# Performance work log

Measured on AMD Instinct MI355X. Metric: run time of the kernel, lower is better.

## Reference

```python
import jax, jax.numpy as jnp
import numpy as np

B, N, L, ND = 512, 4096, 128, 1


def setup_inputs() -> dict:
    key = jax.random.key(0)
    ks = jax.random.split(key, 20)
    g = lambda k, shape, s=0.05: jax.random.normal(k, shape, dtype=jnp.float32) * s
    IN = 3 * L + ND  # MLP input: [mem, mem, delta_t, x]
    inp = {
        "x": jax.random.normal(ks[0], (B, N, ND), jnp.float32),
        "memory": jax.random.normal(ks[1], (N, L), jnp.float32),
        "delta_t": jax.random.normal(ks[2], (B, N, L), jnp.float32),
        "src_w1": g(ks[3], (L, IN)), "src_b1": g(ks[4], (L,)),
        "src_w2": g(ks[5], (L, L)), "src_b2": g(ks[6], (L,)),
        "tar_w1": g(ks[7], (L, IN)), "tar_b1": g(ks[8], (L,)),
        "tar_w2": g(ks[9], (L, L)), "tar_b2": g(ks[10], (L,)),
        "gru_wih": g(ks[11], (3 * L, L)), "gru_whh": g(ks[12], (3 * L, L)),
        "gru_bih": g(ks[13], (3 * L,)), "gru_bhh": g(ks[14], (3 * L,)),
        "source": jax.random.randint(ks[15], (B, 1), 0, N, dtype=jnp.int64),
        "target": jax.random.randint(ks[16], (B, 1), 0, N, dtype=jnp.int64),
    }
    return inp


def _mlp(h, w1, b1, w2, b2):
    return jax.nn.relu(h @ w1.T + b1) @ w2.T + b2


def _gru_cell(inp, h, wih, whh, bih, bhh):
    gi = inp @ wih.T + bih          # [n, 3L]
    gh = h @ whh.T + bhh            # [n, 3L]
    i_r, i_z, i_n = jnp.split(gi, 3, axis=-1)
    h_r, h_z, h_n = jnp.split(gh, 3, axis=-1)
    r = jax.nn.sigmoid(i_r + h_r)
    z = jax.nn.sigmoid(i_z + h_z)
    n = jnp.tanh(i_n + r * h_n)
    return (1.0 - z) * n + z * h


def reference(x, memory, delta_t, src_w1, src_b1, src_w2, src_b2,
              tar_w1, tar_b1, tar_w2, tar_b2,
              gru_wih, gru_whh, gru_bih, gru_bhh, source, target):
    b = x.shape[0]
    bi = jnp.arange(b)
    s = source[:, 0]
    t = target[:, 0]
    src_mem = memory[s]                 # [B, L]
    tar_mem = memory[t]                 # [B, L]
    src_x = x[bi, s, :]                 # [B, ND]
    tar_x = x[bi, t, :]
    src_dt = delta_t[bi, s, :]          # [B, L]
    tar_dt = delta_t[bi, t, :]
    src_in = jnp.concatenate([src_mem, tar_mem, src_dt, src_x], axis=-1)
    tar_in = jnp.concatenate([tar_mem, src_mem, tar_dt, tar_x], axis=-1)
    src_msg = _mlp(src_in, src_w1, src_b1, src_w2, src_b2)
    tar_msg = _mlp(tar_in, tar_w1, tar_b1, tar_w2, tar_b2)

    # unique + scatter_mean == segment-mean over node ids, touching only seen nodes
    ids = jnp.concatenate([s, t], axis=0)                       # [2B]
    msgs = jnp.concatenate([src_msg, tar_msg], axis=0)          # [2B, L]
    n_nodes = memory.shape[0]
    msg_sum = jax.ops.segment_sum(msgs, ids, num_segments=n_nodes)
    cnt = jax.ops.segment_sum(jnp.ones((ids.shape[0],), msgs.dtype), ids,
                              num_segments=n_nodes)
    agg = msg_sum / jnp.maximum(cnt, 1.0)[:, None]              # [N, L]
    new_mem = _gru_cell(agg, memory, gru_wih, gru_whh, gru_bih, gru_bhh)
    seen = (cnt > 0)[:, None]
    return jnp.where(seen, new_mem, memory)
```

## Files before the change

### kernel.cpp

```cpp
#include <hip/hip_runtime.h>
#include <math.h>

#define BB 512
#define NN 4096
#define LL 128
#define IN_DIM 385
#define NK4_1 97
#define NK4_2 32
#define EPB 2
#define GPB 4

#define OFF_MSG   0
#define OFF_CNT   (OFF_MSG + NN * LL)
#define OFF_COUNT (OFF_CNT + NN)
#define OFF_LIST  (OFF_COUNT + 4)
#define OFF_W1PS  529416
#define OFF_W1PT  (OFF_W1PS + NK4_1 * LL * 4)
#define OFF_W2PS  (OFF_W1PT + NK4_1 * LL * 4)
#define OFF_W2PT  (OFF_W2PS + NK4_2 * LL * 4)
#define OFF_WIHP  (OFF_W2PT + NK4_2 * LL * 4)
#define OFF_WHHP  (OFF_WIHP + 3 * NK4_2 * LL * 4)

__global__ __launch_bounds__(256) void prep_kernel(
    const float* __restrict__ sw1, const float* __restrict__ tw1,
    const float* __restrict__ sw2, const float* __restrict__ tw2,
    const float* __restrict__ wih, const float* __restrict__ whh,
    float* __restrict__ ws)
{
    const int i = blockIdx.x * 256 + threadIdx.x;
    const int stride = gridDim.x * 256;

    float4* msg4 = (float4*)(ws + OFF_MSG);
    const float4 z4 = make_float4(0.f, 0.f, 0.f, 0.f);
    for (int idx = i; idx < NN * LL / 4; idx += stride)
        msg4[idx] = z4;
    for (int idx = i; idx < NN; idx += stride)
        ws[OFF_CNT + idx] = 0.0f;
    if (i == 0)
        ((int*)ws)[OFF_COUNT] = 0;

    float4* w1ps = (float4*)(ws + OFF_W1PS);
    float4* w1pt = (float4*)(ws + OFF_W1PT);
    for (int idx = i; idx < NK4_1 * LL; idx += stride) {
        const int k4 = idx >> 7, j = idx & 127;
        const int k = k4 * 4;
        float4 a, b;
        a.x = sw1[j * IN_DIM + k];     b.x = tw1[j * IN_DIM + k];
        a.y = (k + 1 < IN_DIM) ? sw1[j * IN_DIM + k + 1] : 0.f;
        b.y = (k + 1 < IN_DIM) ? tw1[j * IN_DIM + k + 1] : 0.f;
        a.z = (k + 2 < IN_DIM) ? sw1[j * IN_DIM + k + 2] : 0.f;
        b.z = (k + 2 < IN_DIM) ? tw1[j * IN_DIM + k + 2] : 0.f;
        a.w = (k + 3 < IN_DIM) ? sw1[j * IN_DIM + k + 3] : 0.f;
        b.w = (k + 3 < IN_DIM) ? tw1[j * IN_DIM + k + 3] : 0.f;
        w1ps[idx] = a; w1pt[idx] = b;
    }
    float4* w2ps = (float4*)(ws + OFF_W2PS);
    float4* w2pt = (float4*)(ws + OFF_W2PT);
    for (int idx = i; idx < NK4_2 * LL; idx += stride) {
        const int k4 = idx >> 7, j = idx & 127;
        const int k = k4 * 4;
        w2ps[idx] = make_float4(sw2[j * LL + k], sw2[j * LL + k + 1],
                                sw2[j * LL + k + 2], sw2[j * LL + k + 3]);
        w2pt[idx] = make_float4(tw2[j * LL + k], tw2[j * LL + k + 1],
                                tw2[j * LL + k + 2], tw2[j * LL + k + 3]);
    }
    float4* wihp = (float4*)(ws + OFF_WIHP);
    float4* whhp = (float4*)(ws + OFF_WHHP);
    for (int idx = i; idx < 3 * NK4_2 * LL; idx += stride) {
        const int j = idx & 127;
        const int gk = idx >> 7;
        const int gate = gk >> 5, k4 = gk & 31;
        const int row = gate * LL + j, k = k4 * 4;
        wihp[idx] = make_float4(wih[row * LL + k], wih[row * LL + k + 1],
                                wih[row * LL + k + 2], wih[row * LL + k + 3]);
        whhp[idx] = make_float4(whh[row * LL + k], whh[row * LL + k + 1],
                                whh[row * LL + k + 2], whh[row * LL + k + 3]);
    }
}

__global__ __launch_bounds__(256) void edge_msg_kernel(
    const float* __restrict__ x,
    const float* __restrict__ memory,
    const float* __restrict__ delta_t,
    const float* __restrict__ sb1, const float* __restrict__ sb2,
    const float* __restrict__ tb1, const float* __restrict__ tb2,
    const int* __restrict__ source, const int* __restrict__ target,
    float* __restrict__ ws, float* __restrict__ out)
{
    const int tid = threadIdx.x;

    if (blockIdx.x >= 512) {
        const int cb = blockIdx.x - 512;
        float4* out4 = (float4*)out;
        const float4* mem4 = (const float4*)memory;
        for (int idx = cb * 256 + tid; idx < NN * LL / 4; idx += 32 * 256)
            out4[idx] = mem4[idx];
        return;
    }

    const int side  = blockIdx.x & 1;
    const int chunk = blockIdx.x >> 1;
    const int g     = tid >> 7;
    const int j     = tid & 127;

    const int eg0 = chunk * EPB, eg1 = eg0 + 1;
    const int s0 = source[eg0], t0 = target[eg0];
    const int s1 = source[eg1], t1 = target[eg1];
    const int node0  = side ? t0 : s0, other0 = side ? s0 : t0;
    const int node1  = side ? t1 : s1, other1 = side ? s1 : t1;

    __shared__ float h1[LL][EPB];
    __shared__ float part1[2][EPB][LL];
    __shared__ float part2[2][EPB][LL];

    const float4* w1p = (const float4*)(ws + (side ? OFF_W1PT : OFF_W1PS));
    const float4* w2p = (const float4*)(ws + (side ? OFF_W2PT : OFF_W2PS));
    const float* b1  = side ? tb1 : sb1;
    const float* b2  = side ? tb2 : sb2;

    {
        float a0 = 0.f, a1 = 0.f;
        const float* dA = delta_t + ((size_t)eg0 * NN + node0) * LL;
        const float* dB = delta_t + ((size_t)eg1 * NN + node1) * LL;
        if (g == 0) {
            const float* pA = memory + (size_t)node0 * LL;
            const float* pB = memory + (size_t)node1 * LL;
            #pragma unroll 4
            for (int k4 = 0; k4 < 32; ++k4) {
                const float4 w  = w1p[k4 * LL + j];
                const float4 iA = *(const float4*)(pA + 4 * k4);
                const float4 iB = *(const float4*)(pB + 4 * k4);
                a0 = fmaf(w.x, iA.x, a0); a1 = fmaf(w.x, iB.x, a1);
                a0 = fmaf(w.y, iA.y, a0); a1 = fmaf(w.y, iB.y, a1);
                a0 = fmaf(w.z, iA.z, a0); a1 = fmaf(w.z, iB.z, a1);
                a0 = fmaf(w.w, iA.w, a0); a1 = fmaf(w.w, iB.w, a1);
            }
            #pragma unroll 4
            for (int k4 = 64; k4 < 80; ++k4) {
                const float4 w  = w1p[k4 * LL + j];
                const float4 iA = *(const float4*)(dA + 4 * (k4 - 64));
                const float4 iB = *(const float4*)(dB + 4 * (k4 - 64));
                a0 = fmaf(w.x, iA.x, a0); a1 = fmaf(w.x, iB.x, a1);
                a0 = fmaf(w.y, iA.y, a0); a1 = fmaf(w.y, iB.y, a1);
                a0 = fmaf(w.z, iA.z, a0); a1 = fmaf(w.z, iB.z, a1);
                a0 = fmaf(w.w, iA.w, a0); a1 = fmaf(w.w, iB.w, a1);
            }
        } else {
            const float* pA = memory + (size_t)other0 * LL;
            const float* pB = memory + (size_t)other1 * LL;
            #pragma unroll 4
            for (int k4 = 32; k4 < 64; ++k4) {
                const float4 w  = w1p[k4 * LL + j];
                const float4 iA = *(const float4*)(pA + 4 * (k4 - 32));
                const float4 iB = *(const float4*)(pB + 4 * (k4 - 32));
                a0 = fmaf(w.x, iA.x, a0); a1 = fmaf(w.x, iB.x, a1);
                a0 = fmaf(w.y, iA.y, a0); a1 = fmaf(w.y, iB.y, a1);
                a0 = fmaf(w.z, iA.z, a0); a1 = fmaf(w.z, iB.z, a1);
                a0 = fmaf(w.w, iA.w, a0); a1 = fmaf(w.w, iB.w, a1);
            }
            #pragma unroll 4
            for (int k4 = 80; k4 < 96; ++k4) {
                const float4 w  = w1p[k4 * LL + j];
                const float4 iA = *(const float4*)(dA + 4 * (k4 - 64));
                const float4 iB = *(const float4*)(dB + 4 * (k4 - 64));
                a0 = fmaf(w.x, iA.x, a0); a1 = fmaf(w.x, iB.x, a1);
                a0 = fmaf(w.y, iA.y, a0); a1 = fmaf(w.y, iB.y, a1);
                a0 = fmaf(w.z, iA.z, a0); a1 = fmaf(w.z, iB.z, a1);
                a0 = fmaf(w.w, iA.w, a0); a1 = fmaf(w.w, iB.w, a1);
            }
            {
                const float4 w = w1p[96 * LL + j];
                const float xA = x[(size_t)eg0 * NN + node0];
                const float xB = x[(size_t)eg1 * NN + node1];
                a0 = fmaf(w.x, xA, a0);
                a1 = fmaf(w.x, xB, a1);
            }
        }
        part1[g][0][j] = a0;
        part1[g][1][j] = a1;
    }
    __syncthreads();

    h1[j][g] = fmaxf(part1[0][g][j] + part1[1][g][j] + b1[j], 0.0f);
    __syncthreads();

    {
        const int k40 = g * 16, k41 = k40 + 16;
        float a0 = 0.f, a1 = 0.f;
        #pragma unroll 4
        for (int k4 = k40; k4 < k41; ++k4) {
            const float4 w  = w2p[k4 * LL + j];
            const float4 h0 = *(const float4*)&h1[k4 * 4][0];
            const float4 h2 = *(const float4*)&h1[k4 * 4 + 2][0];
            a0 = fmaf(w.x, h0.x, a0); a1 = fmaf(w.x, h0.y, a1);
            a0 = fmaf(w.y, h0.z, a0); a1 = fmaf(w.y, h0.w, a1);
            a0 = fmaf(w.z, h2.x, a0); a1 = fmaf(w.z, h2.y, a1);
            a0 = fmaf(w.w, h2.z, a0); a1 = fmaf(w.w, h2.w, a1);
        }
        part2[g][0][j] = a0;
        part2[g][1][j] = a1;
    }
    __syncthreads();

    {
        const int node = g ? node1 : node0;
        const float m = part2[0][g][j] + part2[1][g][j] + b2[j];
        atomicAdd(ws + OFF_MSG + (size_t)node * LL + j, m);
    }
    if (tid < EPB) {
        const int node = tid ? node1 : node0;
        const float old = atomicAdd(ws + OFF_CNT + node, 1.0f);
        if (old == 0.0f) {
            const int pos = atomicAdd((int*)ws + OFF_COUNT, 1);
            ((int*)ws)[OFF_LIST + pos] = node;
        }
    }
}

__global__ __launch_bounds__(256) void gru_kernel(
    const float* __restrict__ memory,
    const float* __restrict__ bih, const float* __restrict__ bhh,
    const float* __restrict__ ws,
    float* __restrict__ out)
{
    const int tid = threadIdx.x;
    const int g = tid >> 7, j = tid & 127;
    const int scount = ((const int*)ws)[OFF_COUNT];
    const int base = blockIdx.x * GPB;
    if (base >= scount) return;
    const int nact = min(GPB, scount - base);

    __shared__ float gates[6][GPB][LL];
    __shared__ int   nodes_sh[GPB];

    int nd[GPB];
    #pragma unroll
    for (int s = 0; s < GPB; ++s)
        nd[s] = (base + s < scount) ? ((const int*)ws)[OFF_LIST + base + s]
                                    : ((const int*)ws)[OFF_LIST + base];
    if (tid < GPB) nodes_sh[tid] = nd[tid];

    const float* op0; const float* op1; const float* op2; const float* op3;
    float rc0 = 1.f, rc1 = 1.f, rc2 = 1.f, rc3 = 1.f;
    if (g == 0) {
        op0 = ws + OFF_MSG + (size_t)nd[0] * LL;
        op1 = ws + OFF_MSG + (size_t)nd[1] * LL;
        op2 = ws + OFF_MSG + (size_t)nd[2] * LL;
        op3 = ws + OFF_MSG + (size_t)nd[3] * LL;
        rc0 = 1.0f / ws[OFF_CNT + nd[0]];
        rc1 = 1.0f / ws[OFF_CNT + nd[1]];
        rc2 = 1.0f / ws[OFF_CNT + nd[2]];
        rc3 = 1.0f / ws[OFF_CNT + nd[3]];
    } else {
        op0 = memory + (size_t)nd[0] * LL;
        op1 = memory + (size_t)nd[1] * LL;
        op2 = memory + (size_t)nd[2] * LL;
        op3 = memory + (size_t)nd[3] * LL;
    }

    const float4* wp = (const float4*)(ws + (g ? OFF_WHHP : OFF_WIHP));
    float a0[GPB] = {}, a1[GPB] = {}, a2[GPB] = {};
    #pragma unroll 2
    for (int k4 = 0; k4 < NK4_2; ++k4) {
        const float4 w0 = wp[(0 * NK4_2 + k4) * LL + j];
        const float4 w1 = wp[(1 * NK4_2 + k4) * LL + j];
        const float4 w2 = wp[(2 * NK4_2 + k4) * LL + j];
        const float4 v0 = *(const float4*)(op0 + 4 * k4);
        const float4 v1 = *(const float4*)(op1 + 4 * k4);
        const float4 v2 = *(const float4*)(op2 + 4 * k4);
        const float4 v3 = *(const float4*)(op3 + 4 * k4);
        a0[0] = fmaf(w0.x, v0.x, a0[0]); a0[0] = fmaf(w0.y, v0.y, a0[0]);
        a0[0] = fmaf(w0.z, v0.z, a0[0]); a0[0] = fmaf(w0.w, v0.w, a0[0]);
        a1[0] = fmaf(w1.x, v0.x, a1[0]); a1[0] = fmaf(w1.y, v0.y, a1[0]);
        a1[0] = fmaf(w1.z, v0.z, a1[0]); a1[0] = fmaf(w1.w, v0.w, a1[0]);
        a2[0] = fmaf(w2.x, v0.x, a2[0]); a2[0] = fmaf(w2.y, v0.y, a2[0]);
        a2[0] = fmaf(w2.z, v0.z, a2[0]); a2[0] = fmaf(w2.w, v0.w, a2[0]);

        a0[1] = fmaf(w0.x, v1.x, a0[1]); a0[1] = fmaf(w0.y, v1.y, a0[1]);
        a0[1] = fmaf(w0.z, v1.z, a0[1]); a0[1] = fmaf(w0.w, v1.w, a0[1]);
        a1[1] = fmaf(w1.x, v1.x, a1[1]); a1[1] = fmaf(w1.y, v1.y, a1[1]);
        a1[1] = fmaf(w1.z, v1.z, a1[1]); a1[1] = fmaf(w1.w, v1.w, a1[1]);
        a2[1] = fmaf(w2.x, v1.x, a2[1]); a2[1] = fmaf(w2.y, v1.y, a2[1]);
        a2[1] = fmaf(w2.z, v1.z, a2[1]); a2[1] = fmaf(w2.w, v1.w, a2[1]);

        a0[2] = fmaf(w0.x, v2.x, a0[2]); a0[2] = fmaf(w0.y, v2.y, a0[2]);
        a0[2] = fmaf(w0.z, v2.z, a0[2]); a0[2] = fmaf(w0.w, v2.w, a0[2]);
        a1[2] = fmaf(w1.x, v2.x, a1[2]); a1[2] = fmaf(w1.y, v2.y, a1[2]);
        a1[2] = fmaf(w1.z, v2.z, a1[2]); a1[2] = fmaf(w1.w, v2.w, a1[2]);
        a2[2] = fmaf(w2.x, v2.x, a2[2]); a2[2] = fmaf(w2.y, v2.y, a2[2]);
        a2[2] = fmaf(w2.z, v2.z, a2[2]); a2[2] = fmaf(w2.w, v2.w, a2[2]);

        a0[3] = fmaf(w0.x, v3.x, a0[3]); a0[3] = fmaf(w0.y, v3.y, a0[3]);
        a0[3] = fmaf(w0.z, v3.z, a0[3]); a0[3] = fmaf(w0.w, v3.w, a0[3]);
        a1[3] = fmaf(w1.x, v3.x, a1[3]); a1[3] = fmaf(w1.y, v3.y, a1[3]);
        a1[3] = fmaf(w1.z, v3.z, a1[3]); a1[3] = fmaf(w1.w, v3.w, a1[3]);
        a2[3] = fmaf(w2.x, v3.x, a2[3]); a2[3] = fmaf(w2.y, v3.y, a2[3]);
        a2[3] = fmaf(w2.z, v3.z, a2[3]); a2[3] = fmaf(w2.w, v3.w, a2[3]);
    }
    if (g == 0) {
        a0[0] *= rc0; a1[0] *= rc0; a2[0] *= rc0;
        a0[1] *= rc1; a1[1] *= rc1; a2[1] *= rc1;
        a0[2] *= rc2; a1[2] *= rc2; a2[2] *= rc2;
        a0[3] *= rc3; a1[3] *= rc3; a2[3] *= rc3;
    }
    #pragma unroll
    for (int s = 0; s < GPB; ++s) {
        gates[g * 3 + 0][s][j] = a0[s];
        gates[g * 3 + 1][s][j] = a1[s];
        gates[g * 3 + 2][s][j] = a2[s];
    }
    __syncthreads();

    const int total = nact * LL;
    for (int o = tid; o < total; o += 256) {
        const int s = o >> 7, jj = o & 127;
        const int node = nodes_sh[s];
        const float ir = gates[0][s][jj] + bih[jj];
        const float iz = gates[1][s][jj] + bih[LL + jj];
        const float inn = gates[2][s][jj] + bih[2 * LL + jj];
        const float hr = gates[3][s][jj] + bhh[jj];
        const float hz = gates[4][s][jj] + bhh[LL + jj];
        const float hn = gates[5][s][jj] + bhh[2 * LL + jj];
        const float r = 1.0f / (1.0f + __expf(-(ir + hr)));
        const float z = 1.0f / (1.0f + __expf(-(iz + hz)));
        const float n = tanhf(inn + r * hn);
        const float h = memory[(size_t)node * LL + jj];
        out[(size_t)node * LL + jj] = (1.0f - z) * n + z * h;
    }
}

extern "C" void kernel_launch(void* const* d_in, const int* in_sizes, int n_in,
                              void* d_out, int out_size, void* d_ws, size_t ws_size,
                              hipStream_t stream) {
    const float* x        = (const float*)d_in[0];
    const float* memory   = (const float*)d_in[1];
    const float* delta_t  = (const float*)d_in[2];
    const float* src_w1   = (const float*)d_in[3];
    const float* src_b1   = (const float*)d_in[4];
    const float* src_w2   = (const float*)d_in[5];
    const float* src_b2   = (const float*)d_in[6];
    const float* tar_w1   = (const float*)d_in[7];
    const float* tar_b1   = (const float*)d_in[8];
    const float* tar_w2   = (const float*)d_in[9];
    const float* tar_b2   = (const float*)d_in[10];
    const float* gru_wih  = (const float*)d_in[11];
    const float* gru_whh  = (const float*)d_in[12];
    const float* gru_bih  = (const float*)d_in[13];
    const float* gru_bhh  = (const float*)d_in[14];
    const int*   source   = (const int*)d_in[15];
    const int*   target   = (const int*)d_in[16];

    float* out = (float*)d_out;
    float* ws  = (float*)d_ws;

    prep_kernel<<<512, 256, 0, stream>>>(
        src_w1, tar_w1, src_w2, tar_w2, gru_wih, gru_whh, ws);

    edge_msg_kernel<<<544, 256, 0, stream>>>(
        x, memory, delta_t, src_b1, src_b2, tar_b1, tar_b2,
        source, target, ws, out);

    gru_kernel<<<1024 / GPB, 256, 0, stream>>>(
        memory, gru_bih, gru_bhh, ws, out);
}
```

Measured before the change: 35.68 us.

## Widen edge and GRU blocks to 512 threads and move GRU weight packing

Result: slower. 36.80 us (+3.1%).

```diff
diff --git a/kernel.cpp b/kernel.cpp
--- a/kernel.cpp
+++ b/kernel.cpp
@@ -24,7 +24,6 @@
 __global__ __launch_bounds__(256) void prep_kernel(
     const float* __restrict__ sw1, const float* __restrict__ tw1,
     const float* __restrict__ sw2, const float* __restrict__ tw2,
-    const float* __restrict__ wih, const float* __restrict__ whh,
     float* __restrict__ ws)
 {
     const int i = blockIdx.x * 256 + threadIdx.x;
@@ -64,37 +63,46 @@
         w2pt[idx] = make_float4(tw2[j * LL + k], tw2[j * LL + k + 1],
                                 tw2[j * LL + k + 2], tw2[j * LL + k + 3]);
     }
-    float4* wihp = (float4*)(ws + OFF_WIHP);
-    float4* whhp = (float4*)(ws + OFF_WHHP);
-    for (int idx = i; idx < 3 * NK4_2 * LL; idx += stride) {
-        const int j = idx & 127;
-        const int gk = idx >> 7;
-        const int gate = gk >> 5, k4 = gk & 31;
-        const int row = gate * LL + j, k = k4 * 4;
-        wihp[idx] = make_float4(wih[row * LL + k], wih[row * LL + k + 1],
-                                wih[row * LL + k + 2], wih[row * LL + k + 3]);
-        whhp[idx] = make_float4(whh[row * LL + k], whh[row * LL + k + 1],
-                                whh[row * LL + k + 2], whh[row * LL + k + 3]);
-    }
 }
 
-__global__ __launch_bounds__(256) void edge_msg_kernel(
+#define STEP(w, iA, iB)                                   \
+    a0 = fmaf((w).x, (iA).x, a0); a1 = fmaf((w).x, (iB).x, a1); \
+    a0 = fmaf((w).y, (iA).y, a0); a1 = fmaf((w).y, (iB).y, a1); \
+    a0 = fmaf((w).z, (iA).z, a0); a1 = fmaf((w).z, (iB).z, a1); \
+    a0 = fmaf((w).w, (iA).w, a0); a1 = fmaf((w).w, (iB).w, a1);
+
+__global__ __launch_bounds__(512) void edge_msg_kernel(
     const float* __restrict__ x,
     const float* __restrict__ memory,
     const float* __restrict__ delta_t,
     const float* __restrict__ sb1, const float* __restrict__ sb2,
     const float* __restrict__ tb1, const float* __restrict__ tb2,
+    const float* __restrict__ wih, const float* __restrict__ whh,
     const int* __restrict__ source, const int* __restrict__ target,
     float* __restrict__ ws, float* __restrict__ out)
 {
     const int tid = threadIdx.x;
 
     if (blockIdx.x >= 512) {
-        const int cb = blockIdx.x - 512;
-        float4* out4 = (float4*)out;
-        const float4* mem4 = (const float4*)memory;
-        for (int idx = cb * 256 + tid; idx < NN * LL / 4; idx += 32 * 256)
-            out4[idx] = mem4[idx];
+        if (blockIdx.x < 528) {
+            const int cb = blockIdx.x - 512;
+            float4* out4 = (float4*)out;
+            const float4* mem4 = (const float4*)memory;
+            for (int idx = cb * 512 + tid; idx < NN * LL / 4; idx += 16 * 512)
+                out4[idx] = mem4[idx];
+        } else {
+            const int idx = (blockIdx.x - 528) * 512 + tid;
+            const int j = idx & 127;
+            const int gk = idx >> 7;
+            const int gate = gk >> 5, k4 = gk & 31;
+            const int row = gate * LL + j, k = k4 * 4;
+            ((float4*)(ws + OFF_WIHP))[idx] =
+                make_float4(wih[row * LL + k], wih[row * LL + k + 1],
+                            wih[row * LL + k + 2], wih[row * LL + k + 3]);
+            ((float4*)(ws + OFF_WHHP))[idx] =
+                make_float4(whh[row * LL + k], whh[row * LL + k + 1],
+                            whh[row * LL + k + 2], whh[row * LL + k + 3]);
+        }
         return;
     }
 
@@ -110,8 +118,8 @@
     const int node1  = side ? t1 : s1, other1 = side ? s1 : t1;
 
     __shared__ float h1[LL][EPB];
-    __shared__ float part1[2][EPB][LL];
-    __shared__ float part2[2][EPB][LL];
+    __shared__ float part1[4][EPB][LL];
+    __shared__ float part2[4][EPB][LL];
 
     const float4* w1p = (const float4*)(ws + (side ? OFF_W1PT : OFF_W1PS));
     const float4* w2p = (const float4*)(ws + (side ? OFF_W2PT : OFF_W2PS));
@@ -120,60 +128,63 @@
 
     {
         float a0 = 0.f, a1 = 0.f;
+        const float* nA = memory + (size_t)node0 * LL;
+        const float* nB = memory + (size_t)node1 * LL;
+        const float* oA = memory + (size_t)other0 * LL;
+        const float* oB = memory + (size_t)other1 * LL;
         const float* dA = delta_t + ((size_t)eg0 * NN + node0) * LL;
         const float* dB = delta_t + ((size_t)eg1 * NN + node1) * LL;
+
         if (g == 0) {
-            const float* pA = memory + (size_t)node0 * LL;
-            const float* pB = memory + (size_t)node1 * LL;
-            #pragma unroll 4
-            for (int k4 = 0; k4 < 32; ++k4) {
-                const float4 w  = w1p[k4 * LL + j];
-                const float4 iA = *(const float4*)(pA + 4 * k4);
-                const float4 iB = *(const float4*)(pB + 4 * k4);
-                a0 = fmaf(w.x, iA.x, a0); a1 = fmaf(w.x, iB.x, a1);
-                a0 = fmaf(w.y, iA.y, a0); a1 = fmaf(w.y, iB.y, a1);
-                a0 = fmaf(w.z, iA.z, a0); a1 = fmaf(w.z, iB.z, a1);
-                a0 = fmaf(w.w, iA.w, a0); a1 = fmaf(w.w, iB.w, a1);
-            }
-            #pragma unroll 4
-            for (int k4 = 64; k4 < 80; ++k4) {
-                const float4 w  = w1p[k4 * LL + j];
+            #pragma unroll 4
+            for (int k4 = 0; k4 < 24; ++k4) {
+                const float4 w = w1p[k4 * LL + j];
+                const float4 iA = *(const float4*)(nA + 4 * k4);
+                const float4 iB = *(const float4*)(nB + 4 * k4);
+                STEP(w, iA, iB)
+            }
+        } else if (g == 1) {
+            #pragma unroll 4
+            for (int k4 = 24; k4 < 32; ++k4) {
+                const float4 w = w1p[k4 * LL + j];
+                const float4 iA = *(const float4*)(nA + 4 * k4);
+                const float4 iB = *(const float4*)(nB + 4 * k4);
+                STEP(w, iA, iB)
+            }
+            #pragma unroll 4
+            for (int k4 = 32; k4 < 48; ++k4) {
+                const float4 w = w1p[k4 * LL + j];
+                const float4 iA = *(const float4*)(oA + 4 * (k4 - 32));
+                const float4 iB = *(const float4*)(oB + 4 * (k4 - 32));
+                STEP(w, iA, iB)
+            }
+        } else if (g == 2) {
+            #pragma unroll 4
+            for (int k4 = 48; k4 < 64; ++k4) {
+                const float4 w = w1p[k4 * LL + j];
+                const float4 iA = *(const float4*)(oA + 4 * (k4 - 32));
+                const float4 iB = *(const float4*)(oB + 4 * (k4 - 32));
+                STEP(w, iA, iB)
+            }
+            #pragma unroll 4
+            for (int k4 = 64; k4 < 72; ++k4) {
+                const float4 w = w1p[k4 * LL + j];
                 const float4 iA = *(const float4*)(dA + 4 * (k4 - 64));
                 const float4 iB = *(const float4*)(dB + 4 * (k4 - 64));
-                a0 = fmaf(w.x, iA.x, a0); a1 = fmaf(w.x, iB.x, a1);
-                a0 = fmaf(w.y, iA.y, a0); a1 = fmaf(w.y, iB.y, a1);
-                a0 = fmaf(w.z, iA.z, a0); a1 = fmaf(w.z, iB.z, a1);
-                a0 = fmaf(w.w, iA.w, a0); a1 = fmaf(w.w, iB.w, a1);
+                STEP(w, iA, iB)
             }
         } else {
-            const float* pA = memory + (size_t)other0 * LL;
-            const float* pB = memory + (size_t)other1 * LL;
-            #pragma unroll 4
-            for (int k4 = 32; k4 < 64; ++k4) {
-                const float4 w  = w1p[k4 * LL + j];
-                const float4 iA = *(const float4*)(pA + 4 * (k4 - 32));
-                const float4 iB = *(const float4*)(pB + 4 * (k4 - 32));
-                a0 = fmaf(w.x, iA.x, a0); a1 = fmaf(w.x, iB.x, a1);
-                a0 = fmaf(w.y, iA.y, a0); a1 = fmaf(w.y, iB.y, a1);
-                a0 = fmaf(w.z, iA.z, a0); a1 = fmaf(w.z, iB.z, a1);
-                a0 = fmaf(w.w, iA.w, a0); a1 = fmaf(w.w, iB.w, a1);
-            }
-            #pragma unroll 4
-            for (int k4 = 80; k4 < 96; ++k4) {
-                const float4 w  = w1p[k4 * LL + j];
+            #pragma unroll 4
+            for (int k4 = 72; k4 < 96; ++k4) {
+                const float4 w = w1p[k4 * LL + j];
                 const float4 iA = *(const float4*)(dA + 4 * (k4 - 64));
                 const float4 iB = *(const float4*)(dB + 4 * (k4 - 64));
-                a0 = fmaf(w.x, iA.x, a0); a1 = fmaf(w.x, iB.x, a1);
-                a0 = fmaf(w.y, iA.y, a0); a1 = fmaf(w.y, iB.y, a1);
-                a0 = fmaf(w.z, iA.z, a0); a1 = fmaf(w.z, iB.z, a1);
-                a0 = fmaf(w.w, iA.w, a0); a1 = fmaf(w.w, iB.w, a1);
+                STEP(w, iA, iB)
             }
             {
                 const float4 w = w1p[96 * LL + j];
-                const float xA = x[(size_t)eg0 * NN + node0];
-                const float xB = x[(size_t)eg1 * NN + node1];
-                a0 = fmaf(w.x, xA, a0);
-                a1 = fmaf(w.x, xB, a1);
+                a0 = fmaf(w.x, x[(size_t)eg0 * NN + node0], a0);
+                a1 = fmaf(w.x, x[(size_t)eg1 * NN + node1], a1);
             }
         }
         part1[g][0][j] = a0;
@@ -181,11 +192,15 @@
     }
     __syncthreads();
 
-    h1[j][g] = fmaxf(part1[0][g][j] + part1[1][g][j] + b1[j], 0.0f);
+    if (g < EPB) {
+        const float v = part1[0][g][j] + part1[1][g][j]
+                      + part1[2][g][j] + part1[3][g][j] + b1[j];
+        h1[j][g] = fmaxf(v, 0.0f);
+    }
     __syncthreads();
 
     {
-        const int k40 = g * 16, k41 = k40 + 16;
+        const int k40 = g * 8, k41 = k40 + 8;
         float a0 = 0.f, a1 = 0.f;
         #pragma unroll 4
         for (int k4 = k40; k4 < k41; ++k4) {
@@ -202,9 +217,10 @@
     }
     __syncthreads();
 
-    {
+    if (g < EPB) {
         const int node = g ? node1 : node0;
-        const float m = part2[0][g][j] + part2[1][g][j] + b2[j];
+        const float m = part2[0][g][j] + part2[1][g][j]
+                      + part2[2][g][j] + part2[3][g][j] + b2[j];
         atomicAdd(ws + OFF_MSG + (size_t)node * LL + j, m);
     }
     if (tid < EPB) {
@@ -217,20 +233,20 @@
     }
 }
 
-__global__ __launch_bounds__(256) void gru_kernel(
+__global__ __launch_bounds__(512) void gru_kernel(
     const float* __restrict__ memory,
     const float* __restrict__ bih, const float* __restrict__ bhh,
-    const float* __restrict__ ws,
-    float* __restrict__ out)
+    const float* __restrict__ ws, float* __restrict__ out)
 {
     const int tid = threadIdx.x;
     const int g = tid >> 7, j = tid & 127;
+    const int gsel = g >> 1, khalf = g & 1;
     const int scount = ((const int*)ws)[OFF_COUNT];
     const int base = blockIdx.x * GPB;
     if (base >= scount) return;
     const int nact = min(GPB, scount - base);
 
-    __shared__ float gates[6][GPB][LL];
+    __shared__ float gpart[4][3][GPB][LL];
     __shared__ int   nodes_sh[GPB];
 
     int nd[GPB];
@@ -240,87 +256,55 @@
                                     : ((const int*)ws)[OFF_LIST + base];
     if (tid < GPB) nodes_sh[tid] = nd[tid];
 
-    const float* op0; const float* op1; const float* op2; const float* op3;
-    float rc0 = 1.f, rc1 = 1.f, rc2 = 1.f, rc3 = 1.f;
-    if (g == 0) {
-        op0 = ws + OFF_MSG + (size_t)nd[0] * LL;
-        op1 = ws + OFF_MSG + (size_t)nd[1] * LL;
-        op2 = ws + OFF_MSG + (size_t)nd[2] * LL;
-        op3 = ws + OFF_MSG + (size_t)nd[3] * LL;
-        rc0 = 1.0f / ws[OFF_CNT + nd[0]];
-        rc1 = 1.0f / ws[OFF_CNT + nd[1]];
-        rc2 = 1.0f / ws[OFF_CNT + nd[2]];
-        rc3 = 1.0f / ws[OFF_CNT + nd[3]];
-    } else {
-        op0 = memory + (size_t)nd[0] * LL;
-        op1 = memory + (size_t)nd[1] * LL;
-        op2 = memory + (size_t)nd[2] * LL;
-        op3 = memory + (size_t)nd[3] * LL;
-    }
-
-    const float4* wp = (const float4*)(ws + (g ? OFF_WHHP : OFF_WIHP));
+    const float* op[GPB];
+    float rc[GPB] = {1.f, 1.f, 1.f, 1.f};
+    #pragma unroll
+    for (int s = 0; s < GPB; ++s) {
+        if (gsel == 0) {
+            op[s] = ws + OFF_MSG + (size_t)nd[s] * LL;
+            rc[s] = 1.0f / ws[OFF_CNT + nd[s]];
+        } else {
+            op[s] = memory + (size_t)nd[s] * LL;
+        }
+    }
+
+    const float4* wp = (const float4*)(ws + (gsel ? OFF_WHHP : OFF_WIHP));
     float a0[GPB] = {}, a1[GPB] = {}, a2[GPB] = {};
+    const int k40 = khalf * 16;
     #pragma unroll 2
-    for (int k4 = 0; k4 < NK4_2; ++k4) {
+    for (int k4 = k40; k4 < k40 + 16; ++k4) {
         const float4 w0 = wp[(0 * NK4_2 + k4) * LL + j];
         const float4 w1 = wp[(1 * NK4_2 + k4) * LL + j];
         const float4 w2 = wp[(2 * NK4_2 + k4) * LL + j];
-        const float4 v0 = *(const float4*)(op0 + 4 * k4);
-        const float4 v1 = *(const float4*)(op1 + 4 * k4);
-        const float4 v2 = *(const float4*)(op2 + 4 * k4);
-        const float4 v3 = *(const float4*)(op3 + 4 * k4);
-        a0[0] = fmaf(w0.x, v0.x, a0[0]); a0[0] = fmaf(w0.y, v0.y, a0[0]);
-        a0[0] = fmaf(w0.z, v0.z, a0[0]); a0[0] = fmaf(w0.w, v0.w, a0[0]);
-        a1[0] = fmaf(w1.x, v0.x, a1[0]); a1[0] = fmaf(w1.y, v0.y, a1[0]);
-        a1[0] = fmaf(w1.z, v0.z, a1[0]); a1[0] = fmaf(w1.w, v0.w, a1[0]);
-        a2[0] = fmaf(w2.x, v0.x, a2[0]); a2[0] = fmaf(w2.y, v0.y, a2[0]);
-        a2[0] = fmaf(w2.z, v0.z, a2[0]); a2[0] = fmaf(w2.w, v0.w, a2[0]);
-
-        a0[1] = fmaf(w0.x, v1.x, a0[1]); a0[1] = fmaf(w0.y, v1.y, a0[1]);
-        a0[1] = fmaf(w0.z, v1.z, a0[1]); a0[1] = fmaf(w0.w, v1.w, a0[1]);
-        a1[1] = fmaf(w1.x, v1.x, a1[1]); a1[1] = fmaf(w1.y, v1.y, a1[1]);
-        a1[1] = fmaf(w1.z, v1.z, a1[1]); a1[1] = fmaf(w1.w, v1.w, a1[1]);
-        a2[1] = fmaf(w2.x, v1.x, a2[1]); a2[1] = fmaf(w2.y, v1.y, a2[1]);
-        a2[1] = fmaf(w2.z, v1.z, a2[1]); a2[1] = fmaf(w2.w, v1.w, a2[1]);
-
-        a0[2] = fmaf(w0.x, v2.x, a0[2]); a0[2] = fmaf(w0.y, v2.y, a0[2]);
-        a0[2] = fmaf(w0.z, v2.z, a0[2]); a0[2] = fmaf(w0.w, v2.w, a0[2]);
-        a1[2] = fmaf(w1.x, v2.x, a1[2]); a1[2] = fmaf(w1.y, v2.y, a1[2]);
-        a1[2] = fmaf(w1.z, v2.z, a1[2]); a1[2] = fmaf(w1.w, v2.w, a1[2]);
-        a2[2] = fmaf(w2.x, v2.x, a2[2]); a2[2] = fmaf(w2.y, v2.y, a2[2]);
-        a2[2] = fmaf(w2.z, v2.z, a2[2]); a2[2] = fmaf(w2.w, v2.w, a2[2]);
-
-        a0[3] = fmaf(w0.x, v3.x, a0[3]); a0[3] = fmaf(w0.y, v3.y, a0[3]);
-        a0[3] = fmaf(w0.z, v3.z, a0[3]); a0[3] = fmaf(w0.w, v3.w, a0[3]);
-        a1[3] = fmaf(w1.x, v3.x, a1[3]); a1[3] = fmaf(w1.y, v3.y, a1[3]);
-        a1[3] = fmaf(w1.z, v3.z, a1[3]); a1[3] = fmaf(w1.w, v3.w, a1[3]);
-        a2[3] = fmaf(w2.x, v3.x, a2[3]); a2[3] = fmaf(w2.y, v3.y, a2[3]);
-        a2[3] = fmaf(w2.z, v3.z, a2[3]); a2[3] = fmaf(w2.w, v3.w, a2[3]);
-    }
-    if (g == 0) {
-        a0[0] *= rc0; a1[0] *= rc0; a2[0] *= rc0;
-        a0[1] *= rc1; a1[1] *= rc1; a2[1] *= rc1;
-        a0[2] *= rc2; a1[2] *= rc2; a2[2] *= rc2;
-        a0[3] *= rc3; a1[3] *= rc3; a2[3] *= rc3;
+        #pragma unroll
+        for (int s = 0; s < GPB; ++s) {
+            const float4 v = *(const float4*)(op[s] + 4 * k4);
+            a0[s] = fmaf(w0.x, v.x, a0[s]); a0[s] = fmaf(w0.y, v.y, a0[s]);
+            a0[s] = fmaf(w0.z, v.z, a0[s]); a0[s] = fmaf(w0.w, v.w, a0[s]);
+            a1[s] = fmaf(w1.x, v.x, a1[s]); a1[s] = fmaf(w1.y, v.y, a1[s]);
+            a1[s] = fmaf(w1.z, v.z, a1[s]); a1[s] = fmaf(w1.w, v.w, a1[s]);
+            a2[s] = fmaf(w2.x, v.x, a2[s]); a2[s] = fmaf(w2.y, v.y, a2[s]);
+            a2[s] = fmaf(w2.z, v.z, a2[s]); a2[s] = fmaf(w2.w, v.w, a2[s]);
+        }
     }
     #pragma unroll
     for (int s = 0; s < GPB; ++s) {
-        gates[g * 3 + 0][s][j] = a0[s];
-        gates[g * 3 + 1][s][j] = a1[s];
-        gates[g * 3 + 2][s][j] = a2[s];
+        gpart[g][0][s][j] = a0[s] * rc[s];
+        gpart[g][1][s][j] = a1[s] * rc[s];
+        gpart[g][2][s][j] = a2[s] * rc[s];
     }
     __syncthreads();
 
     const int total = nact * LL;
-    for (int o = tid; o < total; o += 256) {
+    for (int o = tid; o < total; o += 512) {
         const int s = o >> 7, jj = o & 127;
         const int node = nodes_sh[s];
-        const float ir = gates[0][s][jj] + bih[jj];
-        const float iz = gates[1][s][jj] + bih[LL + jj];
-        const float inn = gates[2][s][jj] + bih[2 * LL + jj];
-        const float hr = gates[3][s][jj] + bhh[jj];
-        const float hz = gates[4][s][jj] + bhh[LL + jj];
-        const float hn = gates[5][s][jj] + bhh[2 * LL + jj];
+        const float ir = gpart[0][0][s][jj] + gpart[1][0][s][jj] + bih[jj];
+        const float iz = gpart[0][1][s][jj] + gpart[1][1][s][jj] + bih[LL + jj];
+        const float inn = gpart[0][2][s][jj] + gpart[1][2][s][jj] + bih[2 * LL + jj];
+        const float hr = gpart[2][0][s][jj] + gpart[3][0][s][jj] + bhh[jj];
+        const float hz = gpart[2][1][s][jj] + gpart[3][1][s][jj] + bhh[LL + jj];
+        const float hn = gpart[2][2][s][jj] + gpart[3][2][s][jj] + bhh[2 * LL + jj];
         const float r = 1.0f / (1.0f + __expf(-(ir + hr)));
         const float z = 1.0f / (1.0f + __expf(-(iz + hz)));
         const float n = tanhf(inn + r * hn);
@@ -353,13 +337,13 @@
     float* out = (float*)d_out;
     float* ws  = (float*)d_ws;
 
-    prep_kernel<<<512, 256, 0, stream>>>(
-        src_w1, tar_w1, src_w2, tar_w2, gru_wih, gru_whh, ws);
-
-    edge_msg_kernel<<<544, 256, 0, stream>>>(
+    prep_kernel<<<256, 256, 0, stream>>>(
+        src_w1, tar_w1, src_w2, tar_w2, ws);
+
+    edge_msg_kernel<<<552, 512, 0, stream>>>(
         x, memory, delta_t, src_b1, src_b2, tar_b1, tar_b2,
-        source, target, ws, out);
-
-    gru_kernel<<<1024 / GPB, 256, 0, stream>>>(
+        gru_wih, gru_whh, source, target, ws, out);
+
+    gru_kernel<<<1024 / GPB, 512, 0, stream>>>(
         memory, gru_bih, gru_bhh, ws, out);
 }
```
